# Performance work log

Measured on AMD Instinct MI355X. Metric: run time of the kernel, lower is better.

The kernel has to match this reference:

```python
import jax, jax.numpy as jnp
import numpy as np

B, T, D, M = 4, 4096, 1024, 1024
EPS = 1e-6


def _rms_norm(x, w):
    return x * jax.lax.rsqrt(jnp.mean(x * x, axis=-1, keepdims=True) + EPS) * w


def _linrec(xg, r, h0):
    # h_t = x_t + r_t * h_{t-1}  (SRU-style linear recurrence, sqrll_kernel)
    def step(h, inp):
        xt, rt = inp
        h = xt + rt * h
        return h, h
    _, ys = jax.lax.scan(step, h0, (jnp.swapaxes(xg, 0, 1), jnp.swapaxes(r, 0, 1)))
    return jnp.swapaxes(ys, 0, 1)  # [B,T,M]


def setup_inputs() -> dict:
    key = jax.random.key(0)
    ks = jax.random.split(key, 16)
    s = 0.02
    return {
        "x": jax.random.normal(ks[0], (B, T, D), jnp.float32),
        "mem": jnp.zeros((B, M), jnp.float32),
        "norm_w": jnp.ones((D,), jnp.float32),
        "wr_w": jax.random.normal(ks[1], (M, D), jnp.float32) * s,
        "wr_b": jnp.zeros((M,), jnp.float32),
        "wi_w": jax.random.normal(ks[2], (M, D), jnp.float32) * s,
        "wig_w": jax.random.normal(ks[3], (M, D), jnp.float32) * s,
        "wig_b": jnp.zeros((M,), jnp.float32),
        "wog_w": jax.random.normal(ks[4], (M, D), jnp.float32) * s,
        "wog_b": jnp.zeros((M,), jnp.float32),
        "wo_w": jax.random.normal(ks[5], (D, M), jnp.float32) * s,
        "ffnorm_w": jnp.ones((D,), jnp.float32),
        "ffn_wi_w": jax.random.normal(ks[6], (M, D), jnp.float32) * s,
        "ffn_wg_w": jax.random.normal(ks[7], (M, D), jnp.float32) * s,
        "ffn_wg_b": jnp.zeros((M,), jnp.float32),
        "ffn_wo_w": jax.random.normal(ks[8], (D, M), jnp.float32) * s,
    }


def reference(x, mem, norm_w, wr_w, wr_b, wi_w, wig_w, wig_b, wog_w, wog_b,
              wo_w, ffnorm_w, ffn_wi_w, ffn_wg_w, ffn_wg_b, ffn_wo_w):
    # --- sqrll branch ---
    y = _rms_norm(x, norm_w)                                   # [B,T,D]
    ig = jax.nn.sigmoid(jnp.einsum('btd,md->btm', y, wig_w) + wig_b)
    og = jax.nn.sigmoid(jnp.einsum('btd,md->btm', y, wog_w) + wog_b)
    r = jax.nn.sigmoid(jnp.einsum('btd,md->btm', y, wr_w) + wr_b)
    xg = jnp.einsum('btd,md->btm', y, wi_w) * ig               # gated input
    h = _linrec(xg, r, mem)                                    # [B,T,M]
    mem_out = jax.lax.stop_gradient(h[:, -1])
    s = (h / (1.0 + jnp.abs(h))) * og                          # softsign * out gate
    x = x + jnp.einsum('btm,dm->btd', s, wo_w)                 # residual (dropout=0)
    # --- gated FFN branch ---
    z = _rms_norm(x, ffnorm_w)
    ff = jnp.einsum('btd,md->btm', z, ffn_wi_w) * jax.nn.sigmoid(
        jnp.einsum('btd,md->btm', z, ffn_wg_w) + ffn_wg_b)
    x = x + jnp.einsum('btm,dm->btd', ff, ffn_wo_w)
    return (x, mem_out)
```

## Files before the change

### kernel.cpp

```cpp
#include <hip/hip_runtime.h>
#include <stdint.h>


#define R_ROWS 16384
#define DIM    1024
#define MDIM   1024
#define TSEQ   4096
#define NCHUNK 128
#define TCH    32

typedef __attribute__((ext_vector_type(8)))  short  bf16x8;
typedef __attribute__((ext_vector_type(8)))  ushort u16x8;
typedef __attribute__((ext_vector_type(4)))  float  f32x4;
typedef __attribute__((ext_vector_type(16))) float  f32x16;

__device__ __forceinline__ float bf2f(ushort u) {
  union { float f; unsigned int i; } x; x.i = ((unsigned int)u) << 16; return x.f;
}
__device__ __forceinline__ ushort f2bf(float f) {
  union { float f; unsigned int i; } x; x.f = f;
  unsigned int r = x.i + 0x7fffu + ((x.i >> 16) & 1u);
  return (ushort)(r >> 16);
}
__device__ __forceinline__ float sigmoidf_(float x) {
  return 1.0f / (1.0f + __expf(-x));
}
__device__ __forceinline__ void load_lds16(const void* g, void* s) {
  __builtin_amdgcn_global_load_lds(
      (const __attribute__((address_space(1))) void*)g,
      (__attribute__((address_space(3))) void*)s, 16, 0, 0);
}

#define AOFF(s,h) ((((s)*2)+(h))*8192)
#define BOFF(s,h) (49152 + (((s)*2)+(h))*8192)

__global__ __launch_bounds__(256)
void cvt_weights(const float* __restrict__ w0, const float* __restrict__ w1,
                 const float* __restrict__ w2, const float* __restrict__ w3,
                 const float* __restrict__ w4, const float* __restrict__ w5,
                 const float* __restrict__ w6, const float* __restrict__ w7,
                 ushort* __restrict__ dst, ushort* __restrict__ dst2)
{
  const float* src; size_t base; int il; ushort* d = dst;
  switch (blockIdx.y) {
    case 0: src = w0; base = 0;       il = 0; break;
    case 1: src = w1; base = 1048576; il = 0; break;
    case 2: src = w2; base = 2097152; il = 1; break;
    case 3: src = w3; base = 2097152; il = 2; break;
    case 4: src = w4; base = 5242880; il = 1; break;
    case 5: src = w5; base = 5242880; il = 2; break;
    case 6: src = w6; base = 4194304; il = 0; break;
    default: src = w7; base = 0; il = 0; d = dst2; break;
  }
  const int i = blockIdx.x * 256 + threadIdx.x;
  const size_t e = (size_t)i * 4;
  size_t off;
  if (il == 0) off = base + e;
  else {
    const int row = (int)(e >> 10), col = (int)(e & 1023);
    const int nr = ((row >> 7) << 8) + (row & 127) + (il == 2 ? 128 : 0);
    off = base + (size_t)nr * 1024 + col;
  }
  const float4 v = *(const float4*)(src + e);
  ushort4 o; o.x = f2bf(v.x); o.y = f2bf(v.y); o.z = f2bf(v.z); o.w = f2bf(v.w);
  *(ushort4*)(d + off) = o;
}

template<bool IN_F32>
__global__ __launch_bounds__(256)
void rmsnorm_k(const void* __restrict__ xin, const float* __restrict__ w,
               ushort* __restrict__ y)
{
  __shared__ float red[4];
  const int tid = threadIdx.x;
  const int rh = tid >> 7;
  const int rr = tid & 127;
  const int row = blockIdx.x * 2 + rh;
  const size_t base = (size_t)row * DIM + rr * 8;
  float v[8];
  if (IN_F32) {
    const float4 a = *(const float4*)((const float*)xin + base);
    const float4 b = *(const float4*)((const float*)xin + base + 4);
    v[0]=a.x; v[1]=a.y; v[2]=a.z; v[3]=a.w;
    v[4]=b.x; v[5]=b.y; v[6]=b.z; v[7]=b.w;
  } else {
    const u16x8 xv = *(const u16x8*)((const ushort*)xin + base);
#pragma unroll
    for (int i = 0; i < 8; ++i) v[i] = bf2f(xv[i]);
  }
  float ss = 0.f;
#pragma unroll
  for (int i = 0; i < 8; ++i) ss += v[i] * v[i];
  for (int o = 32; o > 0; o >>= 1) ss += __shfl_down(ss, o, 64);
  const int wave = tid >> 6;
  if ((tid & 63) == 0) red[wave] = ss;
  __syncthreads();
  const float sum = red[rh * 2] + red[rh * 2 + 1];
  const float scale = rsqrtf(sum * (1.0f / DIM) + 1e-6f);
  const float4 wa = *(const float4*)(w + rr * 8);
  const float4 wb = *(const float4*)(w + rr * 8 + 4);
  u16x8 o;
  o[0] = f2bf(v[0] * scale * wa.x); o[1] = f2bf(v[1] * scale * wa.y);
  o[2] = f2bf(v[2] * scale * wa.z); o[3] = f2bf(v[3] * scale * wa.w);
  o[4] = f2bf(v[4] * scale * wb.x); o[5] = f2bf(v[5] * scale * wb.y);
  o[6] = f2bf(v[6] * scale * wb.z); o[7] = f2bf(v[7] * scale * wb.w);
  *(u16x8*)(y + base) = o;
}

template<int MODE>
__global__ __launch_bounds__(512, 2)
void gemm8(const ushort* __restrict__ A, const ushort* __restrict__ W,
           const float* __restrict__ bias, const float* __restrict__ auxf,
           const ushort* __restrict__ auxb, ushort* __restrict__ outb,
           float* __restrict__ outf,
           const float* __restrict__ bias2, const float* __restrict__ bias3,
           ushort* __restrict__ outb2, ushort* __restrict__ outb3)
{
  __shared__ __align__(16) ushort lds[81920];
  const int tid  = threadIdx.x;
  const int bm = blockIdx.x, bn = blockIdx.y;
  const int wave = tid >> 6, lane = tid & 63;
  const int wm = wave >> 2, wn = wave & 3;
  const int l31 = lane & 31, lhi = lane >> 5, l7 = lane & 7;

  const ushort* Ab = A + (size_t)bm * (256 * 1024);
  const ushort* Wb = W + (size_t)bn * (256 * 1024);

  f32x16 acc[4][2];
#pragma unroll
  for (int i = 0; i < 4; ++i)
#pragma unroll
    for (int j = 0; j < 2; ++j)
#pragma unroll
      for (int k = 0; k < 16; ++k) acc[i][j][k] = 0.f;

  const int ci0 = tid, ci1 = tid + 512;
  const size_t gs0 = (size_t)(ci0 >> 3) * 1024 + (size_t)(((ci0 & 7) ^ ((ci0 >> 3) & 7)) << 3);
  const size_t gs1 = (size_t)(ci1 >> 3) * 1024 + (size_t)(((ci1 & 7) ^ ((ci1 >> 3) & 7)) << 3);
  auto stage = [&](const ushort* __restrict__ src, int loff) {
    load_lds16(src + gs0, &lds[loff + ci0 * 8]);
    load_lds16(src + gs1, &lds[loff + ci1 * 8]);
  };

  stage(Ab,               AOFF(0,0));
  stage(Ab + 131072,      AOFF(0,1));
  stage(Wb,               BOFF(0,0));
  stage(Wb + 131072,      BOFF(0,1));
  stage(Ab + 64,          AOFF(1,0));
  stage(Ab + 131072 + 64, AOFF(1,1));
  stage(Wb + 64,          BOFF(1,0));
  asm volatile("s_waitcnt vmcnt(6)" ::: "memory");
  __builtin_amdgcn_s_barrier();

  int kt3 = 0;
  for (int kt = 0; kt < 16; ++kt) {
    const ushort* Ah = &lds[AOFF(kt3, wm)];
    const ushort* Bh = &lds[BOFF(kt & 1, wn >> 1)];
    const int kt2s = (kt3 >= 1) ? kt3 - 1 : 2;
    const int brow0 = (wn & 1) * 64;
    bf16x8 bfa[4][2];
#pragma unroll
    for (int q = 0; q < 4; ++q) {
      if (q == 0) {
#pragma unroll
        for (int qq = 0; qq < 4; ++qq)
#pragma unroll
          for (int nt = 0; nt < 2; ++nt)
            bfa[qq][nt] = *(const bf16x8*)
                &Bh[(brow0 + nt * 32 + l31) * 64 +
                    (((qq * 2 + lhi) ^ l7) << 3)];
      }
      bf16x8 af[4];
#pragma unroll
      for (int mt = 0; mt < 4; ++mt)
        af[mt] = *(const bf16x8*)
            &Ah[(mt * 32 + l31) * 64 + (((q * 2 + lhi) ^ l7) << 3)];
      if (q == 0 && kt + 1 < 16)
        stage(Wb + 131072 + (kt + 1) * 64, BOFF((kt + 1) & 1, 1));
      if (q == 1 && kt + 2 < 16)
        stage(Ab + (kt + 2) * 64,          AOFF(kt2s, 0));
      if (q == 2 && kt + 2 < 16)
        stage(Ab + 131072 + (kt + 2) * 64, AOFF(kt2s, 1));
      if (q == 3) {
        if (kt + 2 < 16)
          stage(Wb + (kt + 2) * 64,        BOFF(kt & 1, 0));
        if (kt < 14)       asm volatile("s_waitcnt vmcnt(6)" ::: "memory");
        else if (kt == 14) asm volatile("s_waitcnt vmcnt(0)" ::: "memory");
      }
      __builtin_amdgcn_s_barrier();
      asm volatile("s_waitcnt lgkmcnt(0)" ::: "memory");
      __builtin_amdgcn_s_setprio(1);
#pragma unroll
      for (int mt = 0; mt < 4; ++mt)
#pragma unroll
        for (int nt = 0; nt < 2; ++nt)
          acc[mt][nt] = __builtin_amdgcn_mfma_f32_32x32x16_bf16(
              af[mt], bfa[q][nt], acc[mt][nt], 0, 0, 0);
      __builtin_amdgcn_s_setprio(0);
    }
    kt3 = (kt3 == 2) ? 0 : kt3 + 1;
  }

  __builtin_amdgcn_s_barrier();
  float* C = (float*)lds;
  const bool gated = (MODE == 5) || (MODE == 6 && bn >= 8);
#pragma unroll 1
  for (int h = 0; h < 2; ++h) {
    if (wm == h) {
      const int cb = wn * 64;
#pragma unroll
      for (int mt = 0; mt < 4; ++mt)
#pragma unroll
        for (int nt = 0; nt < 2; ++nt)
#pragma unroll
          for (int rq = 0; rq < 4; ++rq)
#pragma unroll
            for (int rr = 0; rr < 4; ++rr) {
              const int rw = mt * 32 + rr + 8 * rq + 4 * lhi;
              const int cw = cb + nt * 32 + l31;
              C[rw * 256 + cw] = acc[mt][nt][rq * 4 + rr];
            }
    }
    __syncthreads();
    if (gated) {
      const int outcol = (MODE == 6) ? (bn - 8) * 128 : bn * 128;
      const float* bp = (MODE == 6) ? bias3 : bias;
      ushort* ob = (MODE == 6) ? outb3 : outb;
#pragma unroll 1
      for (int sp = 0; sp < 4; ++sp) {
        const int lin = sp * 4096 + tid * 8;
        const int row = lin >> 7, c8 = lin & 127;
        const float4 gA = *(const float4*)&C[row * 256 + c8];
        const float4 gB = *(const float4*)&C[row * 256 + c8 + 4];
        const float4 vA = *(const float4*)&C[row * 256 + c8 + 128];
        const float4 vB = *(const float4*)&C[row * 256 + c8 + 132];
        const float4 b0 = *(const float4*)(bp + outcol + c8);
        const float4 b1 = *(const float4*)(bp + outcol + c8 + 4);
        const int rg = bm * 256 + h * 128 + row;
        const size_t gidx = (size_t)rg * 1024 + outcol + c8;
        u16x8 o;
        o[0] = f2bf(vA.x * sigmoidf_(gA.x + b0.x));
        o[1] = f2bf(vA.y * sigmoidf_(gA.y + b0.y));
        o[2] = f2bf(vA.z * sigmoidf_(gA.z + b0.z));
        o[3] = f2bf(vA.w * sigmoidf_(gA.w + b0.w));
        o[4] = f2bf(vB.x * sigmoidf_(gB.x + b1.x));
        o[5] = f2bf(vB.y * sigmoidf_(gB.y + b1.y));
        o[6] = f2bf(vB.z * sigmoidf_(gB.z + b1.z));
        o[7] = f2bf(vB.w * sigmoidf_(gB.w + b1.w));
        *(u16x8*)(ob + gidx) = o;
      }
    } else {
#pragma unroll 1
      for (int sp = 0; sp < 8; ++sp) {
        const int lin = sp * 4096 + tid * 8;
        const int row = lin >> 8, c8 = lin & 255;
        const float4 vA = *(const float4*)&C[row * 256 + c8];
        const float4 vB = *(const float4*)&C[row * 256 + c8 + 4];
        const int rg = bm * 256 + h * 128 + row;
        if (MODE == 6) {
          const int grp = bn >> 2;
          ushort* ob = grp ? outb2 : outb;
          const float* bp = grp ? bias2 : bias;
          const int colbase = (bn & 3) * 256;
          const size_t gidx = (size_t)rg * 1024 + colbase + c8;
          const float4 b0 = *(const float4*)(bp + colbase + c8);
          const float4 b1 = *(const float4*)(bp + colbase + c8 + 4);
          u16x8 o;
          o[0] = f2bf(sigmoidf_(vA.x + b0.x)); o[1] = f2bf(sigmoidf_(vA.y + b0.y));
          o[2] = f2bf(sigmoidf_(vA.z + b0.z)); o[3] = f2bf(sigmoidf_(vA.w + b0.w));
          o[4] = f2bf(sigmoidf_(vB.x + b1.x)); o[5] = f2bf(sigmoidf_(vB.y + b1.y));
          o[6] = f2bf(sigmoidf_(vB.z + b1.z)); o[7] = f2bf(sigmoidf_(vB.w + b1.w));
          *(u16x8*)(ob + gidx) = o;
        } else if (MODE == 1) {
          const size_t gidx = (size_t)rg * 1024 + bn * 256 + c8;
          const float4 a0 = *(const float4*)(auxf + gidx);
          const float4 a1 = *(const float4*)(auxf + gidx + 4);
          u16x8 o;
          o[0] = f2bf(vA.x + a0.x); o[1] = f2bf(vA.y + a0.y);
          o[2] = f2bf(vA.z + a0.z); o[3] = f2bf(vA.w + a0.w);
          o[4] = f2bf(vB.x + a1.x); o[5] = f2bf(vB.y + a1.y);
          o[6] = f2bf(vB.z + a1.z); o[7] = f2bf(vB.w + a1.w);
          *(u16x8*)(outb + gidx) = o;
        } else {
          const size_t gidx = (size_t)rg * 1024 + bn * 256 + c8;
          const u16x8 a8 = *(const u16x8*)(auxb + gidx);
          float4 o0, o1;
          o0.x = vA.x + bf2f(a8[0]); o0.y = vA.y + bf2f(a8[1]);
          o0.z = vA.z + bf2f(a8[2]); o0.w = vA.w + bf2f(a8[3]);
          o1.x = vB.x + bf2f(a8[4]); o1.y = vB.y + bf2f(a8[5]);
          o1.z = vB.z + bf2f(a8[6]); o1.w = vB.w + bf2f(a8[7]);
          *(float4*)(outf + gidx) = o0;
          *(float4*)(outf + gidx + 4) = o1;
        }
      }
    }
    if (h == 0) __syncthreads();
  }
}

__global__ __launch_bounds__(256)
void linrec_passA(ushort* __restrict__ xg, const ushort* __restrict__ r,
                  float* __restrict__ cL, float* __restrict__ cP)
{
  const int g = blockIdx.x * 256 + threadIdx.x;
  const int m4 = (g & 255) << 2;
  const int bc = g >> 8;
  const int b = bc >> 7, c = bc & 127;
  const size_t base = ((size_t)(b * TSEQ + c * TCH)) * MDIM + m4;
  float h0 = 0.f, h1 = 0.f, h2 = 0.f, h3 = 0.f;
  float p0 = 1.f, p1 = 1.f, p2 = 1.f, p3 = 1.f;
  for (int t = 0; t < TCH; ++t) {
    const size_t idx = base + (size_t)t * MDIM;
    const ushort4 xv = *(const ushort4*)&xg[idx];
    const ushort4 rv = *(const ushort4*)&r[idx];
    const float r0 = bf2f(rv.x), r1 = bf2f(rv.y), r2 = bf2f(rv.z), r3 = bf2f(rv.w);
    h0 = fmaf(r0, h0, bf2f(xv.x)); p0 *= r0;
    h1 = fmaf(r1, h1, bf2f(xv.y)); p1 *= r1;
    h2 = fmaf(r2, h2, bf2f(xv.z)); p2 *= r2;
    h3 = fmaf(r3, h3, bf2f(xv.w)); p3 *= r3;
    ushort4 o; o.x = f2bf(h0); o.y = f2bf(h1); o.z = f2bf(h2); o.w = f2bf(h3);
    *(ushort4*)&xg[idx] = o;
  }
  const size_t cb = (size_t)c * 4096 + b * MDIM + m4;
  float4 L4; L4.x = h0; L4.y = h1; L4.z = h2; L4.w = h3;
  float4 P4; P4.x = p0; P4.y = p1; P4.z = p2; P4.w = p3;
  *(float4*)&cL[cb] = L4;
  *(float4*)&cP[cb] = P4;
}

__global__ __launch_bounds__(64)
void linrec_passB(const float* __restrict__ cL, const float* __restrict__ cP,
                  const float* __restrict__ mem, float* __restrict__ cIn,
                  float* __restrict__ memout)
{
  const int g = blockIdx.x * 64 + threadIdx.x;
  float carry = mem[g];
#pragma unroll 4
  for (int c = 0; c < NCHUNK; ++c) {
    cIn[c * 4096 + g] = carry;
    carry = fmaf(cP[c * 4096 + g], carry, cL[c * 4096 + g]);
  }
  memout[g] = carry;
}

__global__ __launch_bounds__(256)
void linrec_passC(const ushort* __restrict__ L, const ushort* __restrict__ r,
                  const ushort* __restrict__ og, const float* __restrict__ cIn,
                  ushort* __restrict__ s)
{
  const int g = blockIdx.x * 256 + threadIdx.x;
  const int m4 = (g & 255) << 2;
  const int bc = g >> 8;
  const int b = bc >> 7, c = bc & 127;
  const size_t base = ((size_t)(b * TSEQ + c * TCH)) * MDIM + m4;
  const size_t cb = (size_t)c * 4096 + b * MDIM + m4;
  const float4 ci = *(const float4*)&cIn[cb];
  float p0 = 1.f, p1 = 1.f, p2 = 1.f, p3 = 1.f;
  for (int t = 0; t < TCH; ++t) {
    const size_t idx = base + (size_t)t * MDIM;
    const ushort4 rv = *(const ushort4*)&r[idx];
    const ushort4 lv = *(const ushort4*)&L[idx];
    const ushort4 ov = *(const ushort4*)&og[idx];
    p0 *= bf2f(rv.x); p1 *= bf2f(rv.y); p2 *= bf2f(rv.z); p3 *= bf2f(rv.w);
    const float a0 = fmaf(p0, ci.x, bf2f(lv.x));
    const float a1 = fmaf(p1, ci.y, bf2f(lv.y));
    const float a2 = fmaf(p2, ci.z, bf2f(lv.z));
    const float a3 = fmaf(p3, ci.w, bf2f(lv.w));
    ushort4 o;
    o.x = f2bf(a0 / (1.0f + fabsf(a0)) * bf2f(ov.x));
    o.y = f2bf(a1 / (1.0f + fabsf(a1)) * bf2f(ov.y));
    o.z = f2bf(a2 / (1.0f + fabsf(a2)) * bf2f(ov.z));
    o.w = f2bf(a3 / (1.0f + fabsf(a3)) * bf2f(ov.w));
    *(ushort4*)&s[idx] = o;
  }
}

extern "C" void kernel_launch(void* const* d_in, const int* in_sizes, int n_in,
                              void* d_out, int out_size, void* d_ws, size_t ws_size,
                              hipStream_t stream)
{
  const float* x        = (const float*)d_in[0];
  const float* mem      = (const float*)d_in[1];
  const float* norm_w   = (const float*)d_in[2];
  const float* wr_w     = (const float*)d_in[3];
  const float* wr_b     = (const float*)d_in[4];
  const float* wi_w     = (const float*)d_in[5];
  const float* wig_w    = (const float*)d_in[6];
  const float* wig_b    = (const float*)d_in[7];
  const float* wog_w    = (const float*)d_in[8];
  const float* wog_b    = (const float*)d_in[9];
  const float* wo_w     = (const float*)d_in[10];
  const float* ffnorm_w = (const float*)d_in[11];
  const float* ffn_wi_w = (const float*)d_in[12];
  const float* ffn_wg_w = (const float*)d_in[13];
  const float* ffn_wg_b = (const float*)d_in[14];
  const float* ffn_wo_w = (const float*)d_in[15];
  float* outF = (float*)d_out;

  ushort* xgL  = (ushort*)d_out;
  ushort* wbf  = (ushort*)((char*)d_out + 33554432ULL);
  float*  cL   = (float*)((char*)d_out + 48234496ULL);
  float*  cP   = (float*)((char*)d_out + 50331648ULL);
  float*  cIn  = (float*)((char*)d_out + 52428800ULL);
  float*  memoutF = outF + 16777216;

  char* ws = (char*)d_ws;
  ushort* y   = (ushort*)(ws);
  ushort* r   = (ushort*)(ws + 33554432ULL);
  ushort* og  = (ushort*)(ws + 67108864ULL);
  ushort* fwo_bf = (ushort*)(ws + 100663296ULL);
  ushort* s   = y;
  ushort* x1  = og;
  ushort* z   = r;
  ushort* gf  = y;

  cvt_weights<<<dim3(1024, 8), 256, 0, stream>>>(
      wr_w, wog_w, wig_w, wi_w, ffn_wg_w, ffn_wi_w, wo_w, ffn_wo_w,
      wbf, fwo_bf);

  rmsnorm_k<true><<<R_ROWS / 2, 256, 0, stream>>>(x, norm_w, y);
  gemm8<6><<<dim3(64, 16), 512, 0, stream>>>(
      y, wbf, wr_b, nullptr, nullptr, r, nullptr, wog_b, wig_b, og, xgL);
  linrec_passA<<<512, 256, 0, stream>>>(xgL, r, cL, cP);
  linrec_passB<<<64, 64, 0, stream>>>(cL, cP, mem, cIn, memoutF);
  linrec_passC<<<512, 256, 0, stream>>>(xgL, r, og, cIn, s);
  gemm8<1><<<dim3(64, 4), 512, 0, stream>>>(
      s, wbf + 4194304, nullptr, x, nullptr, x1, nullptr,
      nullptr, nullptr, nullptr, nullptr);
  rmsnorm_k<false><<<R_ROWS / 2, 256, 0, stream>>>(x1, ffnorm_w, z);
  gemm8<5><<<dim3(64, 8), 512, 0, stream>>>(
      z, wbf + 5242880, ffn_wg_b, nullptr, nullptr, gf, nullptr,
      nullptr, nullptr, nullptr, nullptr);
  gemm8<3><<<dim3(64, 4), 512, 0, stream>>>(
      gf, fwo_bf, nullptr, nullptr, x1, nullptr, outF,
      nullptr, nullptr, nullptr, nullptr);
}
```

Before: 548.7 us.

## Switch GEMM to 16x16x32 MFMA, swizzle epilogue LDS, halve recurrence chunk length

The GEMM inner loop now uses 16x16x32 bf16 MFMA tiles instead of 32x32x16, with a new fragment load pattern and accumulator layout. The epilogue writes to the LDS staging buffer with an XOR swizzle to reduce bank conflicts. Separately, the chunked linear recurrence uses 256 chunks of 16 steps instead of 128 of 32, which doubles the grid of passes A and C to expose more parallelism. The cost is a longer serial carry scan in pass B and more chunk-carry buffer space, so those buffers are relocated.

```diff
diff --git a/kernel.cpp b/kernel.cpp
--- a/kernel.cpp
+++ b/kernel.cpp
@@ -6,13 +6,12 @@
 #define DIM    1024
 #define MDIM   1024
 #define TSEQ   4096
-#define NCHUNK 128
-#define TCH    32
+#define NCHUNK 256
+#define TCH    16
 
 typedef __attribute__((ext_vector_type(8)))  short  bf16x8;
 typedef __attribute__((ext_vector_type(8)))  ushort u16x8;
 typedef __attribute__((ext_vector_type(4)))  float  f32x4;
-typedef __attribute__((ext_vector_type(16))) float  f32x16;
 
 __device__ __forceinline__ float bf2f(ushort u) {
   union { float f; unsigned int i; } x; x.i = ((unsigned int)u) << 16; return x.f;
@@ -121,18 +120,17 @@
   const int bm = blockIdx.x, bn = blockIdx.y;
   const int wave = tid >> 6, lane = tid & 63;
   const int wm = wave >> 2, wn = wave & 3;
-  const int l31 = lane & 31, lhi = lane >> 5, l7 = lane & 7;
+  const int quad = lane >> 4, l16 = lane & 15;
+  const int axor = l16 & 7;
 
   const ushort* Ab = A + (size_t)bm * (256 * 1024);
   const ushort* Wb = W + (size_t)bn * (256 * 1024);
 
-  f32x16 acc[4][2];
-#pragma unroll
-  for (int i = 0; i < 4; ++i)
-#pragma unroll
-    for (int j = 0; j < 2; ++j)
-#pragma unroll
-      for (int k = 0; k < 16; ++k) acc[i][j][k] = 0.f;
+  f32x4 acc[8][4];
+#pragma unroll
+  for (int i = 0; i < 8; ++i)
+#pragma unroll
+    for (int j = 0; j < 4; ++j) acc[i][j] = (f32x4){0.f, 0.f, 0.f, 0.f};
 
   const int ci0 = tid, ci1 = tid + 512;
   const size_t gs0 = (size_t)(ci0 >> 3) * 1024 + (size_t)(((ci0 & 7) ^ ((ci0 >> 3) & 7)) << 3);
@@ -158,23 +156,26 @@
     const ushort* Bh = &lds[BOFF(kt & 1, wn >> 1)];
     const int kt2s = (kt3 >= 1) ? kt3 - 1 : 2;
     const int brow0 = (wn & 1) * 64;
-    bf16x8 bfa[4][2];
+    bf16x8 bfr[4][2];
 #pragma unroll
     for (int q = 0; q < 4; ++q) {
       if (q == 0) {
 #pragma unroll
-        for (int qq = 0; qq < 4; ++qq)
-#pragma unroll
-          for (int nt = 0; nt < 2; ++nt)
-            bfa[qq][nt] = *(const bf16x8*)
-                &Bh[(brow0 + nt * 32 + l31) * 64 +
-                    (((qq * 2 + lhi) ^ l7) << 3)];
+        for (int j = 0; j < 4; ++j)
+#pragma unroll
+          for (int ks = 0; ks < 2; ++ks)
+            bfr[j][ks] = *(const bf16x8*)
+                &Bh[(brow0 + j * 16 + l16) * 64 +
+                    (((ks * 4 + quad) ^ axor) << 3)];
       }
-      bf16x8 af[4];
-#pragma unroll
-      for (int mt = 0; mt < 4; ++mt)
-        af[mt] = *(const bf16x8*)
-            &Ah[(mt * 32 + l31) * 64 + (((q * 2 + lhi) ^ l7) << 3)];
+      bf16x8 af[2][2];
+#pragma unroll
+      for (int p = 0; p < 2; ++p)
+#pragma unroll
+        for (int ks = 0; ks < 2; ++ks)
+          af[p][ks] = *(const bf16x8*)
+              &Ah[((2 * q + p) * 16 + l16) * 64 +
+                  (((ks * 4 + quad) ^ axor) << 3)];
       if (q == 0 && kt + 1 < 16)
         stage(Wb + 131072 + (kt + 1) * 64, BOFF((kt + 1) & 1, 1));
       if (q == 1 && kt + 2 < 16)
@@ -191,11 +192,13 @@
       asm volatile("s_waitcnt lgkmcnt(0)" ::: "memory");
       __builtin_amdgcn_s_setprio(1);
 #pragma unroll
-      for (int mt = 0; mt < 4; ++mt)
-#pragma unroll
-        for (int nt = 0; nt < 2; ++nt)
-          acc[mt][nt] = __builtin_amdgcn_mfma_f32_32x32x16_bf16(
-              af[mt], bfa[q][nt], acc[mt][nt], 0, 0, 0);
+      for (int p = 0; p < 2; ++p)
+#pragma unroll
+        for (int j = 0; j < 4; ++j)
+#pragma unroll
+          for (int ks = 0; ks < 2; ++ks)
+            acc[2 * q + p][j] = __builtin_amdgcn_mfma_f32_16x16x32_bf16(
+                af[p][ks], bfr[j][ks], acc[2 * q + p][j], 0, 0, 0);
       __builtin_amdgcn_s_setprio(0);
     }
     kt3 = (kt3 == 2) ? 0 : kt3 + 1;
@@ -209,17 +212,15 @@
     if (wm == h) {
       const int cb = wn * 64;
 #pragma unroll
-      for (int mt = 0; mt < 4; ++mt)
-#pragma unroll
-        for (int nt = 0; nt < 2; ++nt)
-#pragma unroll
-          for (int rq = 0; rq < 4; ++rq)
-#pragma unroll
-            for (int rr = 0; rr < 4; ++rr) {
-              const int rw = mt * 32 + rr + 8 * rq + 4 * lhi;
-              const int cw = cb + nt * 32 + l31;
-              C[rw * 256 + cw] = acc[mt][nt][rq * 4 + rr];
-            }
+      for (int i = 0; i < 8; ++i)
+#pragma unroll
+        for (int j = 0; j < 4; ++j)
+#pragma unroll
+          for (int g = 0; g < 4; ++g) {
+            const int rw = i * 16 + quad * 4 + g;
+            const int cw = cb + j * 16 + l16;
+            C[rw * 256 + (cw ^ (((rw >> 2) & 1) << 4))] = acc[i][j][g];
+          }
     }
     __syncthreads();
     if (gated) {
@@ -230,10 +231,13 @@
       for (int sp = 0; sp < 4; ++sp) {
         const int lin = sp * 4096 + tid * 8;
         const int row = lin >> 7, c8 = lin & 127;
-        const float4 gA = *(const float4*)&C[row * 256 + c8];
-        const float4 gB = *(const float4*)&C[row * 256 + c8 + 4];
-        const float4 vA = *(const float4*)&C[row * 256 + c8 + 128];
-        const float4 vB = *(const float4*)&C[row * 256 + c8 + 132];
+        const int xr = ((row >> 2) & 1) << 4;
+        const int cg = c8 ^ xr;
+        const int cv = (c8 + 128) ^ xr;
+        const float4 gA = *(const float4*)&C[row * 256 + cg];
+        const float4 gB = *(const float4*)&C[row * 256 + cg + 4];
+        const float4 vA = *(const float4*)&C[row * 256 + cv];
+        const float4 vB = *(const float4*)&C[row * 256 + cv + 4];
         const float4 b0 = *(const float4*)(bp + outcol + c8);
         const float4 b1 = *(const float4*)(bp + outcol + c8 + 4);
         const int rg = bm * 256 + h * 128 + row;
@@ -254,8 +258,10 @@
       for (int sp = 0; sp < 8; ++sp) {
         const int lin = sp * 4096 + tid * 8;
         const int row = lin >> 8, c8 = lin & 255;
-        const float4 vA = *(const float4*)&C[row * 256 + c8];
-        const float4 vB = *(const float4*)&C[row * 256 + c8 + 4];
+        const int xr = ((row >> 2) & 1) << 4;
+        const int cx = c8 ^ xr;
+        const float4 vA = *(const float4*)&C[row * 256 + cx];
+        const float4 vB = *(const float4*)&C[row * 256 + cx + 4];
         const int rg = bm * 256 + h * 128 + row;
         if (MODE == 6) {
           const int grp = bn >> 2;
@@ -305,7 +311,7 @@
   const int g = blockIdx.x * 256 + threadIdx.x;
   const int m4 = (g & 255) << 2;
   const int bc = g >> 8;
-  const int b = bc >> 7, c = bc & 127;
+  const int b = bc >> 8, c = bc & 255;
   const size_t base = ((size_t)(b * TSEQ + c * TCH)) * MDIM + m4;
   float h0 = 0.f, h1 = 0.f, h2 = 0.f, h3 = 0.f;
   float p0 = 1.f, p1 = 1.f, p2 = 1.f, p3 = 1.f;
@@ -351,7 +357,7 @@
   const int g = blockIdx.x * 256 + threadIdx.x;
   const int m4 = (g & 255) << 2;
   const int bc = g >> 8;
-  const int b = bc >> 7, c = bc & 127;
+  const int b = bc >> 8, c = bc & 255;
   const size_t base = ((size_t)(b * TSEQ + c * TCH)) * MDIM + m4;
   const size_t cb = (size_t)c * 4096 + b * MDIM + m4;
   const float4 ci = *(const float4*)&cIn[cb];
@@ -400,8 +406,8 @@
   ushort* xgL  = (ushort*)d_out;
   ushort* wbf  = (ushort*)((char*)d_out + 33554432ULL);
   float*  cL   = (float*)((char*)d_out + 48234496ULL);
-  float*  cP   = (float*)((char*)d_out + 50331648ULL);
-  float*  cIn  = (float*)((char*)d_out + 52428800ULL);
+  float*  cP   = (float*)((char*)d_out + 52428800ULL);
+  float*  cIn  = (float*)((char*)d_out + 56623104ULL);
   float*  memoutF = outF + 16777216;
 
   char* ws = (char*)d_ws;
@@ -421,9 +427,9 @@
   rmsnorm_k<true><<<R_ROWS / 2, 256, 0, stream>>>(x, norm_w, y);
   gemm8<6><<<dim3(64, 16), 512, 0, stream>>>(
       y, wbf, wr_b, nullptr, nullptr, r, nullptr, wog_b, wig_b, og, xgL);
-  linrec_passA<<<512, 256, 0, stream>>>(xgL, r, cL, cP);
+  linrec_passA<<<1024, 256, 0, stream>>>(xgL, r, cL, cP);
   linrec_passB<<<64, 64, 0, stream>>>(cL, cP, mem, cIn, memoutF);
-  linrec_passC<<<512, 256, 0, stream>>>(xgL, r, og, cIn, s);
+  linrec_passC<<<1024, 256, 0, stream>>>(xgL, r, og, cIn, s);
   gemm8<1><<<dim3(64, 4), 512, 0, stream>>>(
       s, wbf + 4194304, nullptr, x, nullptr, x1, nullptr,
       nullptr, nullptr, nullptr, nullptr);
```

After: 535.9 us. -2.3%, faster.
